# Kernel optimization log

Measured on AMD Instinct MI355X. Metric: run time of the kernel, lower is better.

## Reference

```python
import jax, jax.numpy as jnp
from jax import lax
import numpy as np

L2 = 1.0   # regularization_strength for soft_rank
W1 = 1.0   # weight on (1 - spearman)
W2 = 1.0   # weight on BCE-with-logits


def _isotonic_nondecreasing(y):
    """argmin_{v1<=...<=vn} 0.5||v-y||^2 via the min-max (pool means) formula.
    v_i = max_{j<=i} min_{k>=i} mean(y[j..k]). Same solution (and generic
    gradient) as sequential PAV, but fully vectorized / O(n^2)."""
    n = y.shape[0]
    c = jnp.concatenate([jnp.zeros((1,), y.dtype), jnp.cumsum(y)])  # prefix sums
    j = jnp.arange(n)[:, None]
    k = jnp.arange(n)[None, :]
    length = (k - j + 1).astype(y.dtype)
    M = (c[k + 1] - c[j]) / length                    # mean(y[j..k]) for j<=k
    BIG = jnp.asarray(np.finfo(np.float32).max / 4, y.dtype)
    M = jnp.where(j <= k, M, BIG)                     # mask invalid j>k
    S = lax.cummin(M, axis=1, reverse=True)           # S[j,i] = min_{k>=i} M[j,k]
    V = lax.cummax(S, axis=0)                         # V[i,i] = max_{j<=i} S[j,i]
    return jnp.diagonal(V)


def _isotonic_nonincreasing(y):
    # argmin_{v1>=...>=vn} 0.5||v-y||^2  (what fast_soft_sort's isotonic_l2 solves)
    return -_isotonic_nondecreasing(-y)


def _soft_rank_1d(x, reg):
    """fast_soft_sort soft_rank (L2 regularization, ASCENDING) for a 1D vector:
    projection of x/reg onto the permutahedron of w=[n,...,1]."""
    n = x.shape[0]
    theta = x / reg
    w = jnp.arange(n, 0, -1, dtype=x.dtype)           # [n, n-1, ..., 1]
    perm = jnp.argsort(-theta)                        # descending sort
    s = theta[perm]
    dual = _isotonic_nonincreasing(s - w)
    primal = s - dual
    inv = jnp.argsort(perm)
    return primal[inv]


def setup_inputs() -> dict:
    key = jax.random.key(0)
    k1, k2 = jax.random.split(key)
    y_hat = jax.random.normal(k1, (1, 4096), dtype=jnp.float32)   # logits
    y = jax.random.uniform(k2, (1, 4096), dtype=jnp.float32)      # targets in [0,1]
    return {"y_hat": y_hat, "y": y}


def reference(y_hat, y):
    sr = jax.vmap(lambda v: _soft_rank_1d(v, L2))     # rank each row
    p = sr(y_hat)
    t = sr(y)
    p = p - p.mean()
    p = p / jnp.linalg.norm(p)
    t = t - t.mean()
    t = t / jnp.linalg.norm(t)
    spearman = jnp.sum(p * t)
    # BCEWithLogitsLoss (mean reduction): mean(log(1+exp(x)) - x*y), stable form
    bce = jnp.mean(jnp.logaddexp(0.0, y_hat) - y_hat * y)
    return W1 * (1.0 - spearman) + W2 * bce
```

## Files before the change

### kernel.cpp

```cpp
#include <hip/hip_runtime.h>
#include <math.h>

#define N 4096

__global__ __launch_bounds__(256) void rank_kernel(
        const float* __restrict__ yh, const float* __restrict__ yv,
        float* __restrict__ sA, float* __restrict__ sB,
        int* __restrict__ posA, int* __restrict__ posB) {
    int g = blockIdx.x * 256 + threadIdx.x;
    int elem = g >> 4;
    int k = g & 15;
    int row = elem >> 12;
    int i = elem & (N - 1);
    const float* X = row ? yv : yh;
    float x = X[i];
    const float4* X4 = (const float4*)X;
    int cnt = 0;
    int m0 = k * 64;
#pragma unroll 8
    for (int m = m0; m < m0 + 64; ++m) {
        float4 f = X4[m];
        int j = 4 * m;
        cnt += (int)(f.x > x) | ((int)(f.x == x) & (int)((j + 0) < i));
        cnt += (int)(f.y > x) | ((int)(f.y == x) & (int)((j + 1) < i));
        cnt += (int)(f.z > x) | ((int)(f.z == x) & (int)((j + 2) < i));
        cnt += (int)(f.w > x) | ((int)(f.w == x) & (int)((j + 3) < i));
    }
    cnt += __shfl_xor(cnt, 1, 16);
    cnt += __shfl_xor(cnt, 2, 16);
    cnt += __shfl_xor(cnt, 4, 16);
    cnt += __shfl_xor(cnt, 8, 16);
    if (k == 0) {
        if (row) { posB[i] = cnt; sB[cnt] = x; }
        else     { posA[i] = cnt; sA[cnt] = x; }
    }
}

__global__ __launch_bounds__(1024) void finalize_kernel(
        const float* __restrict__ yh, const float* __restrict__ yv,
        const float* __restrict__ sA, const float* __restrict__ sB,
        const int* __restrict__ posA, const int* __restrict__ posB,
        float* __restrict__ out) {
    __shared__ double wtot[2][8];
    __shared__ double CNsh[2];
    __shared__ unsigned short survX[2][512];
    __shared__ double survY[2][512];
    __shared__ unsigned short gX[2][516];
    __shared__ double gY[2][516];
    __shared__ double gSlope[2][516];
    __shared__ int survCnt[2];
    __shared__ int Hsh[2];
    __shared__ double wred[16][6];

    const int tid  = threadIdx.x;
    const int lane = tid & 63;
    const int wave = tid >> 6;
    const int r    = tid >> 9;
    const int ht   = tid & 511;
    const int hw   = wave & 7;
    const int q0   = ht * 8;

    const float* S = r ? sB : sA;
    float4 sa4 = ((const float4*)S)[2 * ht];
    float4 sb4 = ((const float4*)S)[2 * ht + 1];

    int4 pa4 = ((const int4*)posA)[tid];
    int4 pb4 = ((const int4*)posB)[tid];
    float4 xh = ((const float4*)yh)[tid];
    float4 yt = ((const float4*)yv)[tid];

    float sv[8] = {sa4.x, sa4.y, sa4.z, sa4.w, sb4.x, sb4.y, sb4.z, sb4.w};

    double m[8];
    double acc = 0.0;
#pragma unroll
    for (int j = 0; j < 8; ++j) {
        acc += (double)sv[j] - (double)(N - (q0 + j));
        m[j] = acc;
    }
    double tot = m[7], incl = tot;
#pragma unroll
    for (int d = 1; d < 64; d <<= 1) {
        double t = __shfl_up(incl, d, 64);
        if (lane >= d) incl += t;
    }
    if (lane == 63) wtot[r][hw] = incl;
    if (tid < 2) survCnt[tid] = 0;
    __syncthreads();

    if (tid < 16) {
        int rr = tid >> 3, idx = tid & 7;
        double v = wtot[rr][idx], inc = v;
#pragma unroll
        for (int d = 1; d < 8; d <<= 1) {
            double t = __shfl_up(inc, d, 8);
            if (idx >= d) inc += t;
        }
        wtot[rr][idx] = inc - v;
        if (idx == 7) CNsh[rr] = inc;
    }
    __syncthreads();

    double base = wtot[r][hw] + (incl - tot);
    double CN = CNsh[r];
    double eps = 1e-9 * fabs(CN) + 1e-6;
    const double invN = 1.0 / (double)N;

#pragma unroll
    for (int j = 0; j < 8; ++j) {
        int p = q0 + 1 + j;
        if (p < N) {
            double cp = base + m[j];
            if (cp > CN * ((double)p * invN) - eps) {
                int slot = atomicAdd(&survCnt[r], 1);
                if (slot < 512) { survX[r][slot] = (unsigned short)p; survY[r][slot] = cp; }
            }
        }
    }
    __syncthreads();

    if (ht == 0) {
        int k = survCnt[r]; if (k > 512) k = 512;
        for (int a = 1; a < k; ++a) {
            unsigned short vx = survX[r][a]; double vy = survY[r][a];
            int b = a - 1;
            while (b >= 0 && survX[r][b] > vx) {
                survX[r][b + 1] = survX[r][b]; survY[r][b + 1] = survY[r][b]; --b;
            }
            survX[r][b + 1] = vx; survY[r][b + 1] = vy;
        }
        int cnt = 0;
        int xa = 0, xb = 0; double ya = 0.0, yb = 0.0;
        for (int q = 0; q <= k + 1; ++q) {
            int x; double cy;
            if (q == 0)      { x = 0; cy = 0.0; }
            else if (q <= k) { x = (int)survX[r][q - 1]; cy = survY[r][q - 1]; }
            else             { x = N; cy = CN; }
            while (cnt >= 2) {
                double cr = (double)(xb - xa) * (cy - ya) - (yb - ya) * (double)(x - xa);
                if (cr >= 0.0) {
                    cnt--; xb = xa; yb = ya;
                    if (cnt >= 2) { xa = (int)gX[r][cnt - 2]; ya = gY[r][cnt - 2]; }
                } else break;
            }
            gX[r][cnt] = (unsigned short)x; gY[r][cnt] = cy;
            xa = xb; ya = yb; xb = x; yb = cy;
            cnt++;
        }
        Hsh[r] = cnt;
        for (int q = 0; q + 1 < cnt; ++q)
            gSlope[r][q] = (gY[r][q + 1] - gY[r][q]) /
                           (double)((int)gX[r][q + 1] - (int)gX[r][q]);
    }
    __syncthreads();

    double Sa = 0, Sb = 0, Saa = 0, Sbb = 0, Sab = 0, Bce = 0;
    {
        int HA = Hsh[0], HB = Hsh[1];
        int pa[4] = {pa4.x, pa4.y, pa4.z, pa4.w};
        int pb[4] = {pb4.x, pb4.y, pb4.z, pb4.w};
        float xx[4] = {xh.x, xh.y, xh.z, xh.w};
        float yy[4] = {yt.x, yt.y, yt.z, yt.w};
#pragma unroll
        for (int j = 0; j < 4; ++j) {
            int p = pa[j];
            int a = 0, b2 = HA - 1;
            while (b2 - a > 1) {
                int mm = (a + b2) >> 1;
                if ((int)gX[0][mm] <= p) a = mm; else b2 = mm;
            }
            double dualA = gSlope[0][a];
            p = pb[j];
            a = 0; b2 = HB - 1;
            while (b2 - a > 1) {
                int mm = (a + b2) >> 1;
                if ((int)gX[1][mm] <= p) a = mm; else b2 = mm;
            }
            double dualB = gSlope[1][a];

            double av = (double)xx[j] - dualA - 2048.0;
            double bv = (double)yy[j] - dualB - 2048.0;
            Sa += av; Sb += bv; Saa += av * av; Sbb += bv * bv; Sab += av * bv;
            float x = xx[j];
            float e = __expf(-fabsf(x));
            float bt = fmaxf(x, 0.0f) + __logf(1.0f + e) - x * yy[j];
            Bce += (double)bt;
        }
    }
#pragma unroll
    for (int d = 32; d; d >>= 1) {
        Sa  += __shfl_xor(Sa, d, 64);  Sb  += __shfl_xor(Sb, d, 64);
        Saa += __shfl_xor(Saa, d, 64); Sbb += __shfl_xor(Sbb, d, 64);
        Sab += __shfl_xor(Sab, d, 64); Bce += __shfl_xor(Bce, d, 64);
    }
    if (lane == 0) {
        wred[wave][0] = Sa;  wred[wave][1] = Sb;  wred[wave][2] = Saa;
        wred[wave][3] = Sbb; wred[wave][4] = Sab; wred[wave][5] = Bce;
    }
    __syncthreads();
    if (tid == 0) {
        double sa = 0, sb = 0, saa = 0, sbb = 0, sab = 0, bce = 0;
        for (int w = 0; w < 16; ++w) {
            sa += wred[w][0]; sb += wred[w][1]; saa += wred[w][2];
            sbb += wred[w][3]; sab += wred[w][4]; bce += wred[w][5];
        }
        double n = (double)N;
        double cov = sab - sa * sb / n;
        double va = saa - sa * sa / n;
        double vb = sbb - sb * sb / n;
        double spearman = cov / sqrt(va * vb);
        out[0] = (float)(1.0 - spearman + bce / n);
    }
}

extern "C" void kernel_launch(void* const* d_in, const int* in_sizes, int n_in,
                              void* d_out, int out_size, void* d_ws, size_t ws_size,
                              hipStream_t stream) {
    const float* yh = (const float*)d_in[0];
    const float* yv = (const float*)d_in[1];
    float* out = (float*)d_out;

    float* sA  = (float*)d_ws;
    float* sB  = sA + N;
    int* posA  = (int*)(sB + N);
    int* posB  = posA + N;

    hipLaunchKernelGGL(rank_kernel, dim3(512), dim3(256), 0, stream,
                       yh, yv, sA, sB, posA, posB);
    hipLaunchKernelGGL(finalize_kernel, dim3(1), dim3(1024), 0, stream,
                       yh, yv, sA, sB, posA, posB, out);
}
```

Measured before the change: 77.24 us.

## Compute rank prefix sums in the rank kernel, drop the single-block scan

Each rank thread now also sums the values that rank above its element and derives that element's prefix sum of (sorted value minus weight) in closed form. The finalize kernel therefore reads prefix sums directly instead of scanning the sorted array. The rank kernel splits each element across 32 lanes instead of 16 and launches twice the blocks. This moves the serial scan out of the single-block finalize kernel, but adds double-precision accumulation in the quadratic counting loop and doubles the shuffle reduction work.

New measurement: 79.08 us. 2.4% more time.

```diff
diff --git a/kernel.cpp b/kernel.cpp
--- a/kernel.cpp
+++ b/kernel.cpp
@@ -5,44 +5,54 @@
 
 __global__ __launch_bounds__(256) void rank_kernel(
         const float* __restrict__ yh, const float* __restrict__ yv,
-        float* __restrict__ sA, float* __restrict__ sB,
-        int* __restrict__ posA, int* __restrict__ posB) {
+        int* __restrict__ posA, int* __restrict__ posB,
+        double* __restrict__ csA, double* __restrict__ csB,
+        double* __restrict__ CNg) {
     int g = blockIdx.x * 256 + threadIdx.x;
-    int elem = g >> 4;
-    int k = g & 15;
+    int elem = g >> 5;
+    int k = g & 31;
     int row = elem >> 12;
     int i = elem & (N - 1);
     const float* X = row ? yv : yh;
     float x = X[i];
     const float4* X4 = (const float4*)X;
     int cnt = 0;
-    int m0 = k * 64;
+    double ds = 0.0;
+    int m0 = k * 32;
 #pragma unroll 8
-    for (int m = m0; m < m0 + 64; ++m) {
+    for (int m = m0; m < m0 + 32; ++m) {
         float4 f = X4[m];
         int j = 4 * m;
-        cnt += (int)(f.x > x) | ((int)(f.x == x) & (int)((j + 0) < i));
-        cnt += (int)(f.y > x) | ((int)(f.y == x) & (int)((j + 1) < i));
-        cnt += (int)(f.z > x) | ((int)(f.z == x) & (int)((j + 2) < i));
-        cnt += (int)(f.w > x) | ((int)(f.w == x) & (int)((j + 3) < i));
-    }
-    cnt += __shfl_xor(cnt, 1, 16);
-    cnt += __shfl_xor(cnt, 2, 16);
-    cnt += __shfl_xor(cnt, 4, 16);
-    cnt += __shfl_xor(cnt, 8, 16);
+        int f0 = (int)(f.x > x) | ((int)(f.x == x) & (int)((j + 0) < i));
+        int f1 = (int)(f.y > x) | ((int)(f.y == x) & (int)((j + 1) < i));
+        int f2 = (int)(f.z > x) | ((int)(f.z == x) & (int)((j + 2) < i));
+        int f3 = (int)(f.w > x) | ((int)(f.w == x) & (int)((j + 3) < i));
+        cnt += f0 + f1 + f2 + f3;
+        float s4 = (f0 ? f.x : 0.0f) + (f1 ? f.y : 0.0f)
+                 + (f2 ? f.z : 0.0f) + (f3 ? f.w : 0.0f);
+        ds += (double)s4;
+    }
+#pragma unroll
+    for (int d = 1; d < 32; d <<= 1) {
+        cnt += __shfl_xor(cnt, d, 32);
+        ds  += __shfl_xor(ds, d, 32);
+    }
     if (k == 0) {
-        if (row) { posB[i] = cnt; sB[cnt] = x; }
-        else     { posA[i] = cnt; sA[cnt] = x; }
+        double p = (double)cnt;
+        double C = ds - (p * (double)N - p * (p - 1.0) * 0.5);
+        if (row) { posB[i] = cnt; csB[i] = C; }
+        else     { posA[i] = cnt; csA[i] = C; }
+        if (cnt == N - 1)
+            CNg[row] = ds + (double)x - (double)N * (double)(N + 1) * 0.5;
     }
 }
 
 __global__ __launch_bounds__(1024) void finalize_kernel(
         const float* __restrict__ yh, const float* __restrict__ yv,
-        const float* __restrict__ sA, const float* __restrict__ sB,
         const int* __restrict__ posA, const int* __restrict__ posB,
+        const double* __restrict__ csA, const double* __restrict__ csB,
+        const double* __restrict__ CNg,
         float* __restrict__ out) {
-    __shared__ double wtot[2][8];
-    __shared__ double CNsh[2];
     __shared__ unsigned short survX[2][512];
     __shared__ double survY[2][512];
     __shared__ unsigned short gX[2][516];
@@ -57,63 +67,40 @@
     const int wave = tid >> 6;
     const int r    = tid >> 9;
     const int ht   = tid & 511;
-    const int hw   = wave & 7;
-    const int q0   = ht * 8;
-
-    const float* S = r ? sB : sA;
-    float4 sa4 = ((const float4*)S)[2 * ht];
-    float4 sb4 = ((const float4*)S)[2 * ht + 1];
+
+    const int* P = r ? posB : posA;
+    const double* CS = r ? csB : csA;
+    int4 q4a = ((const int4*)P)[2 * ht];
+    int4 q4b = ((const int4*)P)[2 * ht + 1];
+    double2 c0 = ((const double2*)CS)[4 * ht + 0];
+    double2 c1 = ((const double2*)CS)[4 * ht + 1];
+    double2 c2 = ((const double2*)CS)[4 * ht + 2];
+    double2 c3 = ((const double2*)CS)[4 * ht + 3];
+    double CN = CNg[r];
 
     int4 pa4 = ((const int4*)posA)[tid];
     int4 pb4 = ((const int4*)posB)[tid];
     float4 xh = ((const float4*)yh)[tid];
     float4 yt = ((const float4*)yv)[tid];
 
-    float sv[8] = {sa4.x, sa4.y, sa4.z, sa4.w, sb4.x, sb4.y, sb4.z, sb4.w};
-
-    double m[8];
-    double acc = 0.0;
-#pragma unroll
-    for (int j = 0; j < 8; ++j) {
-        acc += (double)sv[j] - (double)(N - (q0 + j));
-        m[j] = acc;
-    }
-    double tot = m[7], incl = tot;
-#pragma unroll
-    for (int d = 1; d < 64; d <<= 1) {
-        double t = __shfl_up(incl, d, 64);
-        if (lane >= d) incl += t;
-    }
-    if (lane == 63) wtot[r][hw] = incl;
     if (tid < 2) survCnt[tid] = 0;
     __syncthreads();
 
-    if (tid < 16) {
-        int rr = tid >> 3, idx = tid & 7;
-        double v = wtot[rr][idx], inc = v;
-#pragma unroll
-        for (int d = 1; d < 8; d <<= 1) {
-            double t = __shfl_up(inc, d, 8);
-            if (idx >= d) inc += t;
-        }
-        wtot[rr][idx] = inc - v;
-        if (idx == 7) CNsh[rr] = inc;
-    }
-    __syncthreads();
-
-    double base = wtot[r][hw] + (incl - tot);
-    double CN = CNsh[r];
     double eps = 1e-9 * fabs(CN) + 1e-6;
     const double invN = 1.0 / (double)N;
 
-#pragma unroll
-    for (int j = 0; j < 8; ++j) {
-        int p = q0 + 1 + j;
-        if (p < N) {
-            double cp = base + m[j];
-            if (cp > CN * ((double)p * invN) - eps) {
-                int slot = atomicAdd(&survCnt[r], 1);
-                if (slot < 512) { survX[r][slot] = (unsigned short)p; survY[r][slot] = cp; }
+    {
+        int pj[8] = {q4a.x, q4a.y, q4a.z, q4a.w, q4b.x, q4b.y, q4b.z, q4b.w};
+        double cj[8] = {c0.x, c0.y, c1.x, c1.y, c2.x, c2.y, c3.x, c3.y};
+#pragma unroll
+        for (int j = 0; j < 8; ++j) {
+            int p = pj[j];
+            if (p >= 1) {
+                double cp = cj[j];
+                if (cp > CN * ((double)p * invN) - eps) {
+                    int slot = atomicAdd(&survCnt[r], 1);
+                    if (slot < 512) { survX[r][slot] = (unsigned short)p; survY[r][slot] = cp; }
+                }
             }
         }
     }
@@ -220,13 +207,14 @@
     const float* yv = (const float*)d_in[1];
     float* out = (float*)d_out;
 
-    float* sA  = (float*)d_ws;
-    float* sB  = sA + N;
-    int* posA  = (int*)(sB + N);
-    int* posB  = posA + N;
-
-    hipLaunchKernelGGL(rank_kernel, dim3(512), dim3(256), 0, stream,
-                       yh, yv, sA, sB, posA, posB);
+    int* posA   = (int*)d_ws;
+    int* posB   = posA + N;
+    double* csA = (double*)(posB + N);
+    double* csB = csA + N;
+    double* CNg = csB + N;
+
+    hipLaunchKernelGGL(rank_kernel, dim3(1024), dim3(256), 0, stream,
+                       yh, yv, posA, posB, csA, csB, CNg);
     hipLaunchKernelGGL(finalize_kernel, dim3(1), dim3(1024), 0, stream,
-                       yh, yv, sA, sB, posA, posB, out);
+                       yh, yv, posA, posB, csA, csB, CNg, out);
 }
```
